# Kernel optimization log

Hardware: AMD Instinct MI355X
Metric: run time of the kernel (lower is better)

Reference implementation:

```python
import jax, jax.numpy as jnp
import numpy as np

L = 1.0
N = 1024
DT = 1e-7
NUM_STEPS = 128
P = 16  # param_x = param_y
DX = L / (N - 1)


def bilinear_resize(a, n):
    """Bilinear upsample a (P,P) map to (n,n), align_corners=True (matches F.interpolate)."""
    p = a.shape[0]
    coords = jnp.linspace(0.0, p - 1.0, n)
    i0 = jnp.floor(coords).astype(jnp.int32)
    i1 = jnp.minimum(i0 + 1, p - 1)
    w = (coords - i0).astype(a.dtype)
    rows = a[i0] * (1.0 - w)[:, None] + a[i1] * w[:, None]          # (n, p)
    return rows[:, i0] * (1.0 - w)[None, :] + rows[:, i1] * w[None, :]  # (n, n)


def setup_inputs() -> dict:
    key = jax.random.key(0)
    k1, k2, k3 = jax.random.split(key, 3)
    u0 = jax.random.normal(k1, (N, N), dtype=jnp.float32)
    alpha = jax.random.uniform(k2, (P, P), dtype=jnp.float32)
    kappa = jax.random.uniform(k3, (P, P), dtype=jnp.float32)
    return {"u0": u0, "alpha": alpha, "kappa": kappa}


def _simulate(u0, alpha, kappa):
    amap = bilinear_resize(alpha, N)[1:-1, 1:-1]  # interior diffusion coeff
    kmap = bilinear_resize(kappa, N)[1:-1, 1:-1]  # interior advection coeff
    dx2 = DX * DX

    def step(T, _):
        Tc = T[1:-1, 1:-1]
        T_xx = (T[:-2, 1:-1] - 2.0 * Tc + T[2:, 1:-1]) / dx2
        T_yy = (T[1:-1, :-2] - 2.0 * Tc + T[1:-1, 2:]) / dx2
        T_x = (T[2:, 1:-1] - T[:-2, 1:-1]) / (2.0 * DX)
        T_y = (T[1:-1, 2:] - T[1:-1, :-2]) / (2.0 * DX)
        interior = Tc - DT * kmap * (Tc * T_x + Tc * T_y) + DT * amap * (T_xx + T_yy)
        Tn = T.at[1:-1, 1:-1].set(interior)
        # Neumann-like boundary copies, same order as the torch code
        Tn = Tn.at[0, :].set(Tn[1, :])
        Tn = Tn.at[-1, :].set(Tn[-2, :])
        Tn = Tn.at[:, 0].set(Tn[:, 1])
        Tn = Tn.at[:, -1].set(Tn[:, -2])
        return Tn, T  # record the state BEFORE the step (as torch does)

    _, ys = jax.lax.scan(step, u0, None, length=NUM_STEPS)
    return ys[1:]  # (NUM_STEPS-1, N, N)


def reference(u0, alpha, kappa):
    return _simulate(u0, alpha, kappa)
```

## Files before the change

kernel.cpp:

```cpp
#include <hip/hip_runtime.h>

#define GN   1024
#define GNN  (GN * GN)
#define GP   16
#define NOUT 127
#define TILE 64
#define KST  16
#define SZ   96
#define NRB  24
#define NCB  24
#define NTHR 576
#define RST  100
#define AXB  (NRB * 2 * RST)
#define AXS  ((NCB + 1) * RST)
#define PLN  (AXB + 2 * AXS)


__device__ __forceinline__ void coord16(int t, int& c0, int& c1, float& w) {
    double c = (double)t * (15.0 / 1023.0);
    c0 = (int)c;
    c1 = c0 + 1 > 15 ? 15 : c0 + 1;
    w  = (float)(c - (double)c0);
}

__device__ __forceinline__ float bilin16(const float* __restrict__ m,
                                         int i0, int i1, float wi,
                                         int j0, int j1, float wj) {
    float m00 = m[i0 * GP + j0];
    float m10 = m[i1 * GP + j0];
    float m01 = m[i0 * GP + j1];
    float m11 = m[i1 * GP + j1];
    float r0 = m00 * (1.0f - wi) + m10 * wi;
    float r1 = m01 * (1.0f - wi) + m11 * wi;
    return r0 * (1.0f - wj) + r1 * wj;
}

__device__ __forceinline__ float cellv(float C, float L, float R, float U, float D,
                                       float a2, float k2) {
    float s   = (D - U) + (R - L);
    float lap = fmaf(-4.0f, C, (U + D) + (L + R));
    return fmaf(a2, lap, fmaf(-k2, C * s, C));
}

__device__ __forceinline__ float4 rowcell(float4 v, float4 U, float4 D,
                                          float sl, float sr,
                                          float4 a2, float4 k2,
                                          bool isl, bool isr) {
    float L0 = isl ? v.x : sl;
    float C0 = isl ? v.y : v.x;
    float R0 = isl ? v.z : v.y;
    float U0 = isl ? U.y : U.x;
    float D0 = isl ? D.y : D.x;
    float L3 = isr ? v.y : v.z;
    float C3 = isr ? v.z : v.w;
    float R3 = isr ? v.w : sr;
    float U3 = isr ? U.z : U.w;
    float D3 = isr ? D.z : D.w;
    float4 nv;
    nv.x = cellv(C0,  L0,  R0,  U0,  D0,  a2.x, k2.x);
    nv.y = cellv(v.y, v.x, v.z, U.y, D.y, a2.y, k2.y);
    nv.z = cellv(v.z, v.y, v.w, U.z, D.z, a2.z, k2.z);
    nv.w = cellv(C3,  L3,  R3,  U3,  D3,  a2.w, k2.w);
    return nv;
}

__device__ __forceinline__ void lds_barrier() {
    __builtin_amdgcn_sched_barrier(0);
    asm volatile("s_waitcnt lgkmcnt(0)" ::: "memory");
    __builtin_amdgcn_s_barrier();
    __builtin_amdgcn_sched_barrier(0);
}

__global__ __launch_bounds__(256)
void resize_maps_kernel(const float* __restrict__ alpha,
                        const float* __restrict__ kappa,
                        float* __restrict__ a2map,
                        float* __restrict__ k2map) {
    int idx = blockIdx.x * 256 + threadIdx.x;
    if (idx >= GNN) return;
    int i = idx >> 10;
    int j = idx & (GN - 1);
    int ci = i < 1 ? 1 : (i > GN - 2 ? GN - 2 : i);
    int cj = j < 1 ? 1 : (j > GN - 2 ? GN - 2 : j);
    int i0, i1, j0, j1; float wi, wj;
    coord16(ci, i0, i1, wi);
    coord16(cj, j0, j1, wj);
    a2map[idx] = bilin16(alpha, i0, i1, wi, j0, j1, wj) * 0.1046529f;
    k2map[idx] = bilin16(kappa, i0, i1, wi, j0, j1, wj) * 5.115e-5f;
}

template <bool USE_WS>
__global__ __launch_bounds__(NTHR)
void fused_steps_kernel(const float* __restrict__ srcp,
                        const float* __restrict__ Aarg,
                        const float* __restrict__ Karg,
                        float* __restrict__ out,
                        int base)
{
    __shared__ float lds[2][PLN];

    const int tid = threadIdx.x;
    const int rb  = tid / NCB;
    const int cb  = tid - rb * NCB;
    const int r0  = rb * 4;
    const int c4  = cb * 4;

    const int gi0 = blockIdx.y * TILE;
    const int gj0 = blockIdx.x * TILE;
    int oi = gi0 - KST; oi = oi < 0 ? 0 : (oi > GN - SZ ? GN - SZ : oi);
    int oj = gj0 - KST; oj = oj < 0 ? 0 : (oj > GN - SZ ? GN - SZ : oj);
    const int di = gi0 - oi;
    const int dj = gj0 - oj;

    const bool istop = (rb == 0), isbot = (rb == NRB - 1);
    const bool isl   = (cb == 0), isr   = (cb == NCB - 1);
    const bool core  = (rb >= (di >> 2)) && (rb < (di >> 2) + 16)
                    && (cb >= (dj >> 2)) && (cb < (dj >> 2) + 16);
    const int  tmax  = NOUT - base;

    const long gbase = (long)(oi + r0) * GN + oj + c4;

    const int uoff   = (istop ? 0 : (rb * 2 - 1)) * RST + c4;
    const int doff   = (isbot ? (NRB * 2 - 1) : (rb * 2 + 2)) * RST + c4;
    const int w0off  = (rb * 2) * RST + c4;
    const int w3off  = (rb * 2 + 1) * RST + c4;
    const int sloff  = AXB + cb * RST + rb * 4;
    const int wsloff = AXB + (cb + 1) * RST + rb * 4;
    const int sroff  = AXB + AXS + (cb + 1) * RST + rb * 4;
    const int wsroff = AXB + AXS + cb * RST + rb * 4;

    float4 a2[4], k2[4];
    if (USE_WS) {
        #pragma unroll
        for (int q = 0; q < 4; ++q) {
            a2[q] = *(const float4*)(Aarg + gbase + q * GN);
            k2[q] = *(const float4*)(Karg + gbase + q * GN);
        }
    } else {
        #pragma unroll
        for (int q = 0; q < 4; ++q) {
            int gi = oi + r0 + q;
            int ci = gi < 1 ? 1 : (gi > GN - 2 ? GN - 2 : gi);
            int i0, i1; float wi;
            coord16(ci, i0, i1, wi);
            float av[4], kv[4];
            #pragma unroll
            for (int u = 0; u < 4; ++u) {
                int gj = oj + c4 + u;
                int cj = gj < 1 ? 1 : (gj > GN - 2 ? GN - 2 : gj);
                int j0, j1; float wj;
                coord16(cj, j0, j1, wj);
                av[u] = bilin16(Aarg, i0, i1, wi, j0, j1, wj) * 0.1046529f;
                kv[u] = bilin16(Karg, i0, i1, wi, j0, j1, wj) * 5.115e-5f;
            }
            a2[q] = make_float4(av[0], av[1], av[2], av[3]);
            k2[q] = make_float4(kv[0], kv[1], kv[2], kv[3]);
        }
    }

    float4 V[4];
    {
        float4 ld0 = *(const float4*)(srcp + gbase);
        float4 ld1 = *(const float4*)(srcp + gbase + GN);
        float4 ld2 = *(const float4*)(srcp + gbase + 2 * GN);
        float4 ld3 = *(const float4*)(srcp + gbase + 3 * GN);
        *(float4*)&lds[0][w0off]  = ld0;
        *(float4*)&lds[0][w3off]  = ld3;
        *(float4*)&lds[0][wsloff] = make_float4(ld0.w, ld1.w, ld2.w, ld3.w);
        *(float4*)&lds[0][wsroff] = make_float4(ld0.x, ld1.x, ld2.x, ld3.x);
        V[0] = istop ? ld1 : ld0;
        V[1] = ld1;
        V[2] = ld2;
        V[3] = isbot ? ld2 : ld3;
    }
    __syncthreads();

    auto step = [&](const float* __restrict__ cur, float* __restrict__ nxt, int t) {
        float4 U  = *(const float4*)(cur + uoff);
        float4 D  = *(const float4*)(cur + doff);
        float4 SL = *(const float4*)(cur + sloff);
        float4 SR = *(const float4*)(cur + sroff);

        float4 Uop1 = istop ? U : V[0];
        float4 Dop2 = isbot ? D : V[3];

        float4 NV0 = rowcell(V[0], U,    V[1], SL.x, SR.x, a2[0], k2[0], isl, isr);
        float4 NV1 = rowcell(V[1], Uop1, V[2], SL.y, SR.y, a2[1], k2[1], isl, isr);
        float4 NV2 = rowcell(V[2], V[1], Dop2, SL.z, SR.z, a2[2], k2[2], isl, isr);
        float4 NV3 = rowcell(V[3], V[2], D,    SL.w, SR.w, a2[3], k2[3], isl, isr);
        if (istop) NV0 = NV1;
        if (isbot) NV3 = NV2;

        *(float4*)(nxt + w0off)  = NV0;
        *(float4*)(nxt + w3off)  = NV3;
        *(float4*)(nxt + wsloff) = make_float4(NV0.w, NV1.w, NV2.w, NV3.w);
        *(float4*)(nxt + wsroff) = make_float4(NV0.x, NV1.x, NV2.x, NV3.x);

        if (core && t <= tmax) {
            float* slab = out + (long)(base + t - 1) * GNN;
            *(float4*)(slab + gbase)          = NV0;
            *(float4*)(slab + gbase + GN)     = NV1;
            *(float4*)(slab + gbase + 2 * GN) = NV2;
            *(float4*)(slab + gbase + 3 * GN) = NV3;
        }
        V[0] = NV0; V[1] = NV1; V[2] = NV2; V[3] = NV3;
        lds_barrier();
    };

    #pragma unroll 1
    for (int it = 0; it < KST / 2; ++it) {
        step(&lds[0][0], &lds[1][0], 2 * it + 1);
        step(&lds[1][0], &lds[0][0], 2 * it + 2);
    }
}

extern "C" void kernel_launch(void* const* d_in, const int* in_sizes, int n_in,
                              void* d_out, int out_size, void* d_ws, size_t ws_size,
                              hipStream_t stream) {
    const float* u0    = (const float*)d_in[0];
    const float* alpha = (const float*)d_in[1];
    const float* kappa = (const float*)d_in[2];
    float* out = (float*)d_out;

    dim3 grd(GN / TILE, GN / TILE, 1);

    bool use_ws = ws_size >= (size_t)2 * GNN * sizeof(float);

    if (use_ws) {
        float* a2map = (float*)d_ws;
        float* k2map = a2map + GNN;
        resize_maps_kernel<<<(GNN + 255) / 256, 256, 0, stream>>>(alpha, kappa, a2map, k2map);
        for (int b = 0; b < NOUT; b += KST) {
            const float* src = (b == 0) ? u0 : out + (long)(b - 1) * GNN;
            fused_steps_kernel<true><<<grd, NTHR, 0, stream>>>(src, a2map, k2map, out, b);
        }
    } else {
        for (int b = 0; b < NOUT; b += KST) {
            const float* src = (b == 0) ? u0 : out + (long)(b - 1) * GNN;
            fused_steps_kernel<false><<<grd, NTHR, 0, stream>>>(src, alpha, kappa, out, b);
        }
    }
}
```

Before: 212.5 us.

## Use rectangular 64x32 tiles, drop precomputed coefficient maps, hoist state loads

```diff
diff --git a/kernel.cpp b/kernel.cpp
--- a/kernel.cpp
+++ b/kernel.cpp
@@ -4,15 +4,18 @@
 #define GNN  (GN * GN)
 #define GP   16
 #define NOUT 127
-#define TILE 64
-#define KST  16
-#define SZ   96
+#define TI   64
+#define TJ   32
+#define KH   16
+#define SZI  96
+#define SZJ  64
 #define NRB  24
-#define NCB  24
-#define NTHR 576
-#define RST  100
+#define NCB  16
+#define NTHR 384
+#define RST  68
+#define AST  100
 #define AXB  (NRB * 2 * RST)
-#define AXS  ((NCB + 1) * RST)
+#define AXS  ((NCB + 1) * AST)
 #define PLN  (AXB + 2 * AXS)
 
 
@@ -71,51 +74,32 @@
     __builtin_amdgcn_sched_barrier(0);
 }
 
-__global__ __launch_bounds__(256)
-void resize_maps_kernel(const float* __restrict__ alpha,
+__global__ __launch_bounds__(NTHR, 3)
+void fused_steps_kernel(const float* __restrict__ srcp,
+                        const float* __restrict__ alpha,
                         const float* __restrict__ kappa,
-                        float* __restrict__ a2map,
-                        float* __restrict__ k2map) {
-    int idx = blockIdx.x * 256 + threadIdx.x;
-    if (idx >= GNN) return;
-    int i = idx >> 10;
-    int j = idx & (GN - 1);
-    int ci = i < 1 ? 1 : (i > GN - 2 ? GN - 2 : i);
-    int cj = j < 1 ? 1 : (j > GN - 2 ? GN - 2 : j);
-    int i0, i1, j0, j1; float wi, wj;
-    coord16(ci, i0, i1, wi);
-    coord16(cj, j0, j1, wj);
-    a2map[idx] = bilin16(alpha, i0, i1, wi, j0, j1, wj) * 0.1046529f;
-    k2map[idx] = bilin16(kappa, i0, i1, wi, j0, j1, wj) * 5.115e-5f;
-}
-
-template <bool USE_WS>
-__global__ __launch_bounds__(NTHR)
-void fused_steps_kernel(const float* __restrict__ srcp,
-                        const float* __restrict__ Aarg,
-                        const float* __restrict__ Karg,
                         float* __restrict__ out,
                         int base)
 {
     __shared__ float lds[2][PLN];
 
     const int tid = threadIdx.x;
-    const int rb  = tid / NCB;
-    const int cb  = tid - rb * NCB;
+    const int rb  = tid >> 4;
+    const int cb  = tid & (NCB - 1);
     const int r0  = rb * 4;
     const int c4  = cb * 4;
 
-    const int gi0 = blockIdx.y * TILE;
-    const int gj0 = blockIdx.x * TILE;
-    int oi = gi0 - KST; oi = oi < 0 ? 0 : (oi > GN - SZ ? GN - SZ : oi);
-    int oj = gj0 - KST; oj = oj < 0 ? 0 : (oj > GN - SZ ? GN - SZ : oj);
+    const int gi0 = blockIdx.y * TI;
+    const int gj0 = blockIdx.x * TJ;
+    int oi = gi0 - KH; oi = oi < 0 ? 0 : (oi > GN - SZI ? GN - SZI : oi);
+    int oj = gj0 - KH; oj = oj < 0 ? 0 : (oj > GN - SZJ ? GN - SZJ : oj);
     const int di = gi0 - oi;
     const int dj = gj0 - oj;
 
     const bool istop = (rb == 0), isbot = (rb == NRB - 1);
     const bool isl   = (cb == 0), isr   = (cb == NCB - 1);
-    const bool core  = (rb >= (di >> 2)) && (rb < (di >> 2) + 16)
-                    && (cb >= (dj >> 2)) && (cb < (dj >> 2) + 16);
+    const bool core  = (rb >= (di >> 2)) && (rb < (di >> 2) + TI / 4)
+                    && (cb >= (dj >> 2)) && (cb < (dj >> 2) + TJ / 4);
     const int  tmax  = NOUT - base;
 
     const long gbase = (long)(oi + r0) * GN + oj + c4;
@@ -124,19 +108,25 @@
     const int doff   = (isbot ? (NRB * 2 - 1) : (rb * 2 + 2)) * RST + c4;
     const int w0off  = (rb * 2) * RST + c4;
     const int w3off  = (rb * 2 + 1) * RST + c4;
-    const int sloff  = AXB + cb * RST + rb * 4;
-    const int wsloff = AXB + (cb + 1) * RST + rb * 4;
-    const int sroff  = AXB + AXS + (cb + 1) * RST + rb * 4;
-    const int wsroff = AXB + AXS + cb * RST + rb * 4;
+    const int sloff  = AXB + cb * AST + r0;
+    const int wsloff = AXB + (cb + 1) * AST + r0;
+    const int sroff  = AXB + AXS + (cb + 1) * AST + r0;
+    const int wsroff = AXB + AXS + cb * AST + r0;
+
+    float4 ld0 = *(const float4*)(srcp + gbase);
+    float4 ld1 = *(const float4*)(srcp + gbase + GN);
+    float4 ld2 = *(const float4*)(srcp + gbase + 2 * GN);
+    float4 ld3 = *(const float4*)(srcp + gbase + 3 * GN);
 
     float4 a2[4], k2[4];
-    if (USE_WS) {
+    {
+        int j0[4], j1[4]; float wj[4];
         #pragma unroll
-        for (int q = 0; q < 4; ++q) {
-            a2[q] = *(const float4*)(Aarg + gbase + q * GN);
-            k2[q] = *(const float4*)(Karg + gbase + q * GN);
+        for (int u = 0; u < 4; ++u) {
+            int gj = oj + c4 + u;
+            int cj = gj < 1 ? 1 : (gj > GN - 2 ? GN - 2 : gj);
+            coord16(cj, j0[u], j1[u], wj[u]);
         }
-    } else {
         #pragma unroll
         for (int q = 0; q < 4; ++q) {
             int gi = oi + r0 + q;
@@ -146,71 +136,63 @@
             float av[4], kv[4];
             #pragma unroll
             for (int u = 0; u < 4; ++u) {
-                int gj = oj + c4 + u;
-                int cj = gj < 1 ? 1 : (gj > GN - 2 ? GN - 2 : gj);
-                int j0, j1; float wj;
-                coord16(cj, j0, j1, wj);
-                av[u] = bilin16(Aarg, i0, i1, wi, j0, j1, wj) * 0.1046529f;
-                kv[u] = bilin16(Karg, i0, i1, wi, j0, j1, wj) * 5.115e-5f;
+                av[u] = bilin16(alpha, i0, i1, wi, j0[u], j1[u], wj[u]) * 0.1046529f;
+                kv[u] = bilin16(kappa, i0, i1, wi, j0[u], j1[u], wj[u]) * 5.115e-5f;
             }
             a2[q] = make_float4(av[0], av[1], av[2], av[3]);
             k2[q] = make_float4(kv[0], kv[1], kv[2], kv[3]);
         }
     }
 
+    *(float4*)&lds[0][w0off]  = ld0;
+    *(float4*)&lds[0][w3off]  = ld3;
+    *(float4*)&lds[0][wsloff] = make_float4(ld0.w, ld1.w, ld2.w, ld3.w);
+    *(float4*)&lds[0][wsroff] = make_float4(ld0.x, ld1.x, ld2.x, ld3.x);
     float4 V[4];
-    {
-        float4 ld0 = *(const float4*)(srcp + gbase);
-        float4 ld1 = *(const float4*)(srcp + gbase + GN);
-        float4 ld2 = *(const float4*)(srcp + gbase + 2 * GN);
-        float4 ld3 = *(const float4*)(srcp + gbase + 3 * GN);
-        *(float4*)&lds[0][w0off]  = ld0;
-        *(float4*)&lds[0][w3off]  = ld3;
-        *(float4*)&lds[0][wsloff] = make_float4(ld0.w, ld1.w, ld2.w, ld3.w);
-        *(float4*)&lds[0][wsroff] = make_float4(ld0.x, ld1.x, ld2.x, ld3.x);
-        V[0] = istop ? ld1 : ld0;
-        V[1] = ld1;
-        V[2] = ld2;
-        V[3] = isbot ? ld2 : ld3;
-    }
+    V[0] = istop ? ld1 : ld0;
+    V[1] = ld1;
+    V[2] = ld2;
+    V[3] = isbot ? ld2 : ld3;
     __syncthreads();
 
-    auto step = [&](const float* __restrict__ cur, float* __restrict__ nxt, int t) {
-        float4 U  = *(const float4*)(cur + uoff);
-        float4 D  = *(const float4*)(cur + doff);
-        float4 SL = *(const float4*)(cur + sloff);
-        float4 SR = *(const float4*)(cur + sroff);
-
-        float4 Uop1 = istop ? U : V[0];
-        float4 Dop2 = isbot ? D : V[3];
-
-        float4 NV0 = rowcell(V[0], U,    V[1], SL.x, SR.x, a2[0], k2[0], isl, isr);
-        float4 NV1 = rowcell(V[1], Uop1, V[2], SL.y, SR.y, a2[1], k2[1], isl, isr);
-        float4 NV2 = rowcell(V[2], V[1], Dop2, SL.z, SR.z, a2[2], k2[2], isl, isr);
-        float4 NV3 = rowcell(V[3], V[2], D,    SL.w, SR.w, a2[3], k2[3], isl, isr);
-        if (istop) NV0 = NV1;
-        if (isbot) NV3 = NV2;
-
-        *(float4*)(nxt + w0off)  = NV0;
-        *(float4*)(nxt + w3off)  = NV3;
-        *(float4*)(nxt + wsloff) = make_float4(NV0.w, NV1.w, NV2.w, NV3.w);
-        *(float4*)(nxt + wsroff) = make_float4(NV0.x, NV1.x, NV2.x, NV3.x);
-
-        if (core && t <= tmax) {
-            float* slab = out + (long)(base + t - 1) * GNN;
-            *(float4*)(slab + gbase)          = NV0;
-            *(float4*)(slab + gbase + GN)     = NV1;
-            *(float4*)(slab + gbase + 2 * GN) = NV2;
-            *(float4*)(slab + gbase + 3 * GN) = NV3;
+    #pragma unroll 1
+    for (int it = 0; it < KH / 2; ++it) {
+        #pragma unroll
+        for (int half = 0; half < 2; ++half) {
+            const int t = 2 * it + 1 + half;
+            const float* cur = half ? &lds[1][0] : &lds[0][0];
+            float*       nxt = half ? &lds[0][0] : &lds[1][0];
+
+            float4 U  = *(const float4*)(cur + uoff);
+            float4 D  = *(const float4*)(cur + doff);
+            float4 SL = *(const float4*)(cur + sloff);
+            float4 SR = *(const float4*)(cur + sroff);
+
+            float4 Uop1 = istop ? U : V[0];
+            float4 Dop2 = isbot ? D : V[3];
+
+            float4 NV0 = rowcell(V[0], U,    V[1], SL.x, SR.x, a2[0], k2[0], isl, isr);
+            float4 NV1 = rowcell(V[1], Uop1, V[2], SL.y, SR.y, a2[1], k2[1], isl, isr);
+            float4 NV2 = rowcell(V[2], V[1], Dop2, SL.z, SR.z, a2[2], k2[2], isl, isr);
+            float4 NV3 = rowcell(V[3], V[2], D,    SL.w, SR.w, a2[3], k2[3], isl, isr);
+            if (istop) NV0 = NV1;
+            if (isbot) NV3 = NV2;
+
+            *(float4*)(nxt + w0off)  = NV0;
+            *(float4*)(nxt + w3off)  = NV3;
+            *(float4*)(nxt + wsloff) = make_float4(NV0.w, NV1.w, NV2.w, NV3.w);
+            *(float4*)(nxt + wsroff) = make_float4(NV0.x, NV1.x, NV2.x, NV3.x);
+
+            if (core && t <= tmax) {
+                float* slab = out + (long)(base + t - 1) * GNN;
+                *(float4*)(slab + gbase)          = NV0;
+                *(float4*)(slab + gbase + GN)     = NV1;
+                *(float4*)(slab + gbase + 2 * GN) = NV2;
+                *(float4*)(slab + gbase + 3 * GN) = NV3;
+            }
+            V[0] = NV0; V[1] = NV1; V[2] = NV2; V[3] = NV3;
+            lds_barrier();
         }
-        V[0] = NV0; V[1] = NV1; V[2] = NV2; V[3] = NV3;
-        lds_barrier();
-    };
-
-    #pragma unroll 1
-    for (int it = 0; it < KST / 2; ++it) {
-        step(&lds[0][0], &lds[1][0], 2 * it + 1);
-        step(&lds[1][0], &lds[0][0], 2 * it + 2);
     }
 }
 
@@ -222,22 +204,11 @@
     const float* kappa = (const float*)d_in[2];
     float* out = (float*)d_out;
 
-    dim3 grd(GN / TILE, GN / TILE, 1);
-
-    bool use_ws = ws_size >= (size_t)2 * GNN * sizeof(float);
-
-    if (use_ws) {
-        float* a2map = (float*)d_ws;
-        float* k2map = a2map + GNN;
-        resize_maps_kernel<<<(GNN + 255) / 256, 256, 0, stream>>>(alpha, kappa, a2map, k2map);
-        for (int b = 0; b < NOUT; b += KST) {
-            const float* src = (b == 0) ? u0 : out + (long)(b - 1) * GNN;
-            fused_steps_kernel<true><<<grd, NTHR, 0, stream>>>(src, a2map, k2map, out, b);
-        }
-    } else {
-        for (int b = 0; b < NOUT; b += KST) {
-            const float* src = (b == 0) ? u0 : out + (long)(b - 1) * GNN;
-            fused_steps_kernel<false><<<grd, NTHR, 0, stream>>>(src, alpha, kappa, out, b);
-        }
+    dim3 grd(GN / TJ, GN / TI, 1);
+    dim3 blk(NTHR, 1, 1);
+
+    for (int b = 0; b < NOUT; b += KH) {
+        const float* src = (b == 0) ? u0 : out + (long)(b - 1) * GNN;
+        fused_steps_kernel<<<grd, blk, 0, stream>>>(src, alpha, kappa, out, b);
     }
 }
```

Result: slower. 247.4 us (+16.4%).
